# Optimization experiments

Measured on AMD Instinct MI355X. Metric: run time of the kernel, lower is better.

The kernel has to match this reference:

```python
import jax, jax.numpy as jnp
import numpy as np

D_MODEL = 1024
N_HEADS = 16
D_HEAD = D_MODEL // N_HEADS


def setup_inputs() -> dict:
    key = jax.random.key(0)
    ks = jax.random.split(key, 11)
    B, S = 2, 2048
    scale = 1.0 / np.sqrt(D_MODEL)
    inp = {
        "query": jax.random.normal(ks[0], (B, S, D_MODEL), jnp.float32),
        "key": jax.random.normal(ks[1], (B, S, D_MODEL), jnp.float32),
        "value": jax.random.normal(ks[2], (B, S, D_MODEL), jnp.float32),
        "Wq": jax.random.normal(ks[3], (D_MODEL, D_MODEL), jnp.float32) * scale,
        "bq": jnp.zeros((D_MODEL,), jnp.float32),
        "Wk": jax.random.normal(ks[4], (D_MODEL, D_MODEL), jnp.float32) * scale,
        "bk": jnp.zeros((D_MODEL,), jnp.float32),
        "Wv": jax.random.normal(ks[5], (D_MODEL, D_MODEL), jnp.float32) * scale,
        "bv": jnp.zeros((D_MODEL,), jnp.float32),
        "Wo": jax.random.normal(ks[6], (D_MODEL, D_MODEL), jnp.float32) * scale,
        "bo": jnp.zeros((D_MODEL,), jnp.float32),
    }
    return inp


def _split_heads(x):
    B, S, _ = x.shape
    return x.reshape(B, S, N_HEADS, D_HEAD).transpose(0, 2, 1, 3)  # [B,H,S,Dh]


def reference(query, key, value, Wq, bq, Wk, bk, Wv, bv, Wo, bo):
    q = _split_heads(query @ Wq + bq)
    k = _split_heads(key @ Wk + bk)
    v = _split_heads(value @ Wv + bv)
    # scores [B,H,S,S] -- faithfully materialized as in the original
    scores = jnp.einsum("bhqd,bhkd->bhqk", q, k) / np.sqrt(D_HEAD)
    attn = jax.nn.softmax(scores, axis=-1)
    out = jnp.einsum("bhqk,bhkd->bhqd", attn, v)  # [B,H,S,Dh]
    B, H, S, Dh = out.shape
    out = out.transpose(0, 2, 1, 3).reshape(B, S, H * Dh)
    return out @ Wo + bo
```

## Files before the change

kernel.cpp:

```cpp
#include <hip/hip_runtime.h>
#include <hip/hip_bf16.h>

using bf16 = __hip_bfloat16;
typedef __bf16 bf16x8 __attribute__((ext_vector_type(8)));
typedef __bf16 bf16x2v __attribute__((ext_vector_type(2)));
typedef float f32x4 __attribute__((ext_vector_type(4)));
typedef float f32x16 __attribute__((ext_vector_type(16)));

#define SEQ 2048
#define DM  1024
#define QSCALE 0.18033688011112042f

__device__ __forceinline__ f32x4 mfma16(bf16x8 a, bf16x8 b, f32x4 c) {
  return __builtin_amdgcn_mfma_f32_16x16x32_bf16(a, b, c, 0, 0, 0);
}
__device__ __forceinline__ f32x16 mfma32(bf16x8 a, bf16x8 b, f32x16 c) {
  return __builtin_amdgcn_mfma_f32_32x32x16_bf16(a, b, c, 0, 0, 0);
}
__device__ __forceinline__ void gload16(const void* g, void* l) {
  __builtin_amdgcn_global_load_lds(
      (const __attribute__((address_space(1))) unsigned int*)g,
      (__attribute__((address_space(3))) unsigned int*)l, 16, 0, 0);
}
__device__ __forceinline__ unsigned short bfbits(float x) {
  bf16 h = __float2bfloat16(x);
  return *reinterpret_cast<unsigned short*>(&h);
}
__device__ __forceinline__ unsigned pk2(float a, float b) {
#if __has_builtin(__builtin_amdgcn_cvt_pk_bf16_f32)
  bf16x2v r = __builtin_amdgcn_cvt_pk_bf16_f32(a, b);
  return *reinterpret_cast<unsigned*>(&r);
#else
  return (unsigned)bfbits(a) | ((unsigned)bfbits(b) << 16);
#endif
}
__device__ __forceinline__ float fexp2(float x) {
#if __has_builtin(__builtin_amdgcn_exp2f)
  return __builtin_amdgcn_exp2f(x);
#else
  return exp2f(x);
#endif
}
__device__ __forceinline__ void plswap(unsigned& a, unsigned& b) {
  asm("v_permlane32_swap_b32 %0, %1" : "+v"(a), "+v"(b));
}

__global__ __launch_bounds__(256) void cast_all(const float* __restrict__ q,
                                                const float* __restrict__ k,
                                                const float* __restrict__ v,
                                                const float* __restrict__ Wq,
                                                const float* __restrict__ Wk,
                                                const float* __restrict__ Wv,
                                                const float* __restrict__ Wo,
                                                bf16* __restrict__ Lx,
                                                bf16* __restrict__ Lw,
                                                bf16* __restrict__ Lwo) {
  __shared__ alignas(16) unsigned char sm[33024];
  const int t = threadIdx.x;
  if (blockIdx.y < 3) {
    const float* src = blockIdx.y == 0 ? q : (blockIdx.y == 1 ? k : v);
    const float* base = src + (size_t)blockIdx.x * 16 * 1024;
    bf16* dst = Lx + (size_t)blockIdx.y * (4096ull * 1024) + (size_t)blockIdx.x * 16384;
    bf16* const xs = (bf16*)sm;
#pragma unroll
    for (int i = 0; i < 16; ++i) {
      int u = t + i * 256;
      int row = u >> 8, c4 = u & 255;
      float4 a = *(const float4*)(base + (size_t)row * 1024 + c4 * 4);
      uint2 o;
      o.x = pk2(a.x, a.y);
      o.y = pk2(a.z, a.w);
      *(uint2*)&xs[row * 1032 + c4 * 4] = o;
    }
    __syncthreads();
#pragma unroll
    for (int i = 0; i < 8; ++i) {
      int u = t + i * 256;
      int k32 = u >> 6, l = u & 63;
      const bf16* p = &xs[(l & 15) * 1032 + k32 * 32 + (l >> 4) * 8];
      *(uint4*)(dst + (size_t)u * 8) = *(const uint4*)p;
    }
    return;
  }
  const int widx = blockIdx.y - 3;
  const float* W = widx == 0 ? Wq : (widx == 1 ? Wk : (widx == 2 ? Wv : Wo));
  bf16* dst = widx < 3 ? (Lw + (size_t)widx * 1048576) : Lwo;
  float* const tf = (float*)sm;
  const int bx = blockIdx.x & 15, by = blockIdx.x >> 4;
#pragma unroll
  for (int i = 0; i < 4; ++i) {
    int u = t + i * 256, r = u >> 4, c4 = u & 15;
    *(float4*)&tf[r * 68 + c4 * 4] = *(const float4*)(W + (size_t)(by * 64 + r) * 1024 + bx * 64 + c4 * 4);
  }
  __syncthreads();
#pragma unroll
  for (int i = 0; i < 2; ++i) {
    int u = t + i * 256;
    int sub = u >> 6, l = u & 63;
    int n16l = sub >> 1, k32l = sub & 1;
    int nn = n16l * 16 + (l & 15);
    int kk = k32l * 32 + (l >> 4) * 8;
    alignas(16) unsigned o[4];
#pragma unroll
    for (int p = 0; p < 4; ++p) o[p] = pk2(tf[(kk + 2 * p) * 68 + nn], tf[(kk + 2 * p + 1) * 68 + nn]);
    size_t off = ((((size_t)(bx * 4 + n16l)) * 32 + (by * 2 + k32l)) * 64 + l) * 8;
    *(uint4*)(dst + off) = *(const uint4*)o;
  }
}

__global__ __launch_bounds__(512, 4) void qkv_gemm(const bf16* __restrict__ Lw,
                                                   const bf16* __restrict__ Lx,
                                                   const float* __restrict__ bq,
                                                   const float* __restrict__ bk,
                                                   const float* __restrict__ bv,
                                                   bf16* __restrict__ Lq,
                                                   bf16* __restrict__ Lk,
                                                   bf16* __restrict__ Lv) {
  __shared__ alignas(16) bf16 At[2][8192];
  __shared__ alignas(16) bf16 Bt[2][4096];
  const int t = threadIdx.x, lane = t & 63, w = t >> 6;
  const int m16 = lane & 15, g4 = lane >> 4;
  const int bid = blockIdx.x;
  const int logical = (bid & 7) * 48 + (bid >> 3);
  const int third = logical >> 7;
  const int r = logical & 127;
  const int shift = third < 2 ? 5 : 3;
  const int mt = r >> shift, nt = r & ((1 << shift) - 1);
  const int wm = w >> 1, wn = w & 1;
  const bf16* Wb = Lw + (size_t)third * 1048576;
  const bf16* Xb = Lx + (size_t)third * (4096ull * 1024);
  const bf16* Asrc = third < 2 ? Wb : Xb;
  const bf16* Bsrc = third < 2 ? Xb : Wb;
  f32x4 acc[4][4] = {};

#pragma unroll
  for (int ii = 0; ii < 3; ++ii) {
    int u = w * 3 + ii;
    if (u < 16)
      gload16(Asrc + (((size_t)(mt * 16 + u) * 32 + 0) * 64 + lane) * 8, (void*)&At[0][u * 512]);
    else
      gload16(Bsrc + (((size_t)(nt * 8 + u - 16) * 32 + 0) * 64 + lane) * 8, (void*)&Bt[0][(u - 16) * 512]);
  }

  int cur = 0;
  for (int k = 0; k < 32; ++k) {
    __builtin_amdgcn_s_barrier();
    __builtin_amdgcn_sched_barrier(0);
    if (k < 31) {
      const int nb = cur ^ 1;
#pragma unroll
      for (int ii = 0; ii < 3; ++ii) {
        int u = w * 3 + ii;
        if (u < 16)
          gload16(Asrc + (((size_t)(mt * 16 + u) * 32 + k + 1) * 64 + lane) * 8, (void*)&At[nb][u * 512]);
        else
          gload16(Bsrc + (((size_t)(nt * 8 + u - 16) * 32 + k + 1) * 64 + lane) * 8,
                  (void*)&Bt[nb][(u - 16) * 512]);
      }
      asm volatile("s_waitcnt vmcnt(3)" ::: "memory");
    } else {
      asm volatile("s_waitcnt vmcnt(0)" ::: "memory");
    }
    __builtin_amdgcn_sched_barrier(0);
    __builtin_amdgcn_s_barrier();
    __builtin_amdgcn_sched_barrier(0);

    bf16x8 afr[4], bfr[4];
#pragma unroll
    for (int i = 0; i < 4; ++i) afr[i] = *(const bf16x8*)&At[cur][(wm * 4 + i) * 512 + lane * 8];
#pragma unroll
    for (int j = 0; j < 4; ++j) bfr[j] = *(const bf16x8*)&Bt[cur][(wn * 4 + j) * 512 + lane * 8];
    __builtin_amdgcn_s_setprio(1);
#pragma unroll
    for (int i = 0; i < 4; ++i)
#pragma unroll
      for (int j = 0; j < 4; ++j) acc[i][j] = mfma16(afr[i], bfr[j], acc[i][j]);
    __builtin_amdgcn_s_setprio(0);
    cur ^= 1;
  }

  if (third < 2) {
    bf16* dst = third == 0 ? Lq : Lk;
    const float* bias = third == 0 ? bq : bk;
    const float sc = third == 0 ? QSCALE : 1.0f;
#pragma unroll
    for (int mi = 0; mi < 4; ++mi) {
      int doutb = mt * 256 + wm * 64 + mi * 16 + g4 * 4;
      float4 b4 = *(const float4*)(bias + doutb);
      int hh = doutb >> 6, d32 = (doutb & 63) >> 5;
      int lhi = (doutb & 31) >> 3, half = g4 & 1;
#pragma unroll
      for (int nj = 0; nj < 4; ++nj) {
        int seq = nt * 128 + wn * 64 + nj * 16 + m16;
        int bb2 = seq >> 11, s16w = (seq & 2047) >> 4;
        size_t off = ((((size_t)(bb2 * 128 + s16w)) * 16 + hh) * 2 + d32) * 512 + (m16 + 16 * lhi) * 8 + half * 4;
        uint2 pv;
        pv.x = pk2((acc[mi][nj][0] + b4.x) * sc, (acc[mi][nj][1] + b4.y) * sc);
        pv.y = pk2((acc[mi][nj][2] + b4.z) * sc, (acc[mi][nj][3] + b4.w) * sc);
        *(uint2*)(dst + off) = pv;
      }
    }
  } else {
#pragma unroll
    for (int nj = 0; nj < 4; ++nj) {
      int dout = nt * 128 + wn * 64 + nj * 16 + m16;
      float bvv = bv[dout];
      int hh = dout >> 6, dt = (dout & 63) >> 4;
#pragma unroll
      for (int mi = 0; mi < 4; ++mi) {
        int seqb = mt * 256 + wm * 64 + mi * 16 + g4 * 4;
        int b_ = seqb >> 11, kt = (seqb & 2047) >> 6, ks32 = (seqb & 63) >> 5;
        int lhi = (seqb & 31) >> 3, half = g4 & 1;
        size_t off = (((((size_t)(b_ * 32 + kt)) * 16 + hh) * 4 + dt) * 2 + ks32) * 512 + (m16 + 16 * lhi) * 8 + half * 4;
        uint2 pv;
        pv.x = pk2(acc[mi][nj][0] + bvv, acc[mi][nj][1] + bvv);
        pv.y = pk2(acc[mi][nj][2] + bvv, acc[mi][nj][3] + bvv);
        *(uint2*)(Lv + off) = pv;
      }
    }
  }
}

__global__ __launch_bounds__(512, 4) void flash(const bf16* __restrict__ Lq,
                                                const bf16* __restrict__ Lk,
                                                const bf16* __restrict__ Lv,
                                                bf16* __restrict__ Lab) {
  __shared__ alignas(16) unsigned char smem[65536];
  bf16* const Kb = (bf16*)smem;
  bf16* const Vb = (bf16*)(smem + 32768);

  const int t = threadIdx.x, lane = t & 63, w = t >> 6;
  const int l31 = lane & 31, m16 = lane & 15, hi = lane >> 5, b4 = (lane >> 4) & 1;
  const int qw = w >> 1, g = w & 1, wg = w >> 1;
  const int bid = blockIdx.x;
  const int logical = ((bid & 7) << 6) | (bid >> 3);
  const int qt = logical & 15, h = (logical >> 4) & 15, b = logical >> 8;

  bf16x8 qf[4];
  {
    const int sQ = b * 128 + qt * 8 + qw * 2 + b4;
#pragma unroll
    for (int ks = 0; ks < 4; ++ks) {
      const int d32 = ks >> 1, g4q = (ks & 1) * 2 + hi;
      qf[ks] = *(const bf16x8*)(Lq + (((size_t)sQ * 16 + h) * 2 + d32) * 512 + (m16 + 16 * g4q) * 8);
    }
  }

  const int ss = wg >> 1, sd = wg & 1;
#pragma unroll
  for (int u = 0; u < 2; ++u) {
    const bf16* gk = Lk + ((((size_t)(b * 128 + g * 64 + u * 2 + ss)) * 16 + h) * 2 + sd) * 512 + lane * 8;
    gload16(gk, (void*)(Kb + (g * 2 + 0) * 4096 + u * 2048 + wg * 512));
    const bf16* gv = Lv + (((((size_t)(b * 32 + g * 16)) * 16 + h) * 4 + wg) * 2 + u) * 512 + lane * 8;
    gload16(gv, (void*)(Vb + (g * 2 + 0) * 4096 + u * 2048 + wg * 512));
  }

  float lrow = 0.f;
  f32x16 oacc[2] = {};
  __syncthreads();

  for (int it = 0; it < 16; ++it) {
    const int cur = it & 1;
    const bf16* const Klb = Kb + (g * 2 + cur) * 4096;
    const bf16* const Vlb = Vb + (g * 2 + cur) * 4096;
    if (it < 15) {
      const int nb = cur ^ 1;
#pragma unroll
      for (int u = 0; u < 2; ++u) {
        const int kc = (it + 1) * 2 + u;
        const bf16* gk = Lk + ((((size_t)(b * 128 + g * 64 + kc * 2 + ss)) * 16 + h) * 2 + sd) * 512 + lane * 8;
        gload16(gk, (void*)(Kb + (g * 2 + nb) * 4096 + u * 2048 + wg * 512));
        const bf16* gv = Lv + (((((size_t)(b * 32 + g * 16 + (kc >> 1))) * 16 + h) * 4 + wg) * 2 + (kc & 1)) * 512 + lane * 8;
        gload16(gv, (void*)(Vb + (g * 2 + nb) * 4096 + u * 2048 + wg * 512));
      }
    }

    f32x16 s0 = {}, s1 = {};
    __builtin_amdgcn_s_setprio(1);
#pragma unroll
    for (int ks = 0; ks < 4; ++ks) {
      const int d32 = ks >> 1, g4k = (ks & 1) * 2 + hi;
      bf16x8 kf = *(const bf16x8*)&Klb[((b4 * 2 + d32) * 64 + m16 + 16 * g4k) * 8];
      s0 = mfma32(kf, qf[ks], s0);
    }
#pragma unroll
    for (int ks = 0; ks < 4; ++ks) {
      const int d32 = ks >> 1, g4k = (ks & 1) * 2 + hi;
      bf16x8 kf = *(const bf16x8*)&Klb[2048 + ((b4 * 2 + d32) * 64 + m16 + 16 * g4k) * 8];
      s1 = mfma32(kf, qf[ks], s1);
    }
    __builtin_amdgcn_s_setprio(0);

#pragma unroll
    for (int u = 0; u < 2; ++u) {
      const bf16* const Vl = Vlb + u * 2048;
      const f32x16& s = u == 0 ? s0 : s1;
      float e[16];
#pragma unroll
      for (int r = 0; r < 16; ++r) e[r] = fexp2(s[r]);
      {
        float a0 = e[0] + e[1], a1 = e[2] + e[3], a2 = e[4] + e[5], a3 = e[6] + e[7];
        float a4 = e[8] + e[9], a5 = e[10] + e[11], a6 = e[12] + e[13], a7 = e[14] + e[15];
        lrow += ((a0 + a1) + (a2 + a3)) + ((a4 + a5) + (a6 + a7));
      }
      bf16x8 bP[2];
#pragma unroll
      for (int c = 0; c < 2; ++c) {
        unsigned P0 = pk2(e[8 * c + 0], e[8 * c + 1]);
        unsigned P1 = pk2(e[8 * c + 2], e[8 * c + 3]);
        unsigned P2 = pk2(e[8 * c + 4], e[8 * c + 5]);
        unsigned P3 = pk2(e[8 * c + 6], e[8 * c + 7]);
        plswap(P0, P2);
        plswap(P1, P3);
        alignas(16) unsigned pw[4] = {P0, P1, P2, P3};
        bP[c] = *(const bf16x8*)pw;
      }
      __builtin_amdgcn_s_setprio(1);
#pragma unroll
      for (int dtile = 0; dtile < 2; ++dtile) {
        const int dt = dtile * 2 + b4;
#pragma unroll
        for (int c = 0; c < 2; ++c) {
          bf16x8 av = *(const bf16x8*)&Vl[(dt * 64 + m16 + 16 * (2 * c + hi)) * 8];
          oacc[dtile] = mfma32(av, bP[c], oacc[dtile]);
        }
      }
      __builtin_amdgcn_s_setprio(0);
    }
    __syncthreads();
  }

  lrow += __shfl_xor(lrow, 32);

  float* const Os = (float*)smem;
  float* const Ls = (float*)(smem + 32768);
  if (g == 1) {
#pragma unroll
    for (int dtile = 0; dtile < 2; ++dtile)
#pragma unroll
      for (int r = 0; r < 16; ++r)
        Os[((qw * 2 + dtile) * 16 + r) * 64 + lane] = oacc[dtile][r];
    if (hi == 0) Ls[qw * 32 + l31] = lrow;
  }
  __syncthreads();
  if (g == 0) {
    const float inv = 1.f / (lrow + Ls[qw * 32 + l31]);
    const int sQ = b * 128 + qt * 8 + qw * 2 + b4;
#pragma unroll
    for (int dtile = 0; dtile < 2; ++dtile) {
      const int k32 = h * 2 + dtile;
#pragma unroll
      for (int j = 0; j < 8; ++j) {
        const int r = 2 * j;
        float o0 = oacc[dtile][r] + Os[((qw * 2 + dtile) * 16 + r) * 64 + lane];
        float o1 = oacc[dtile][r + 1] + Os[((qw * 2 + dtile) * 16 + r + 1) * 64 + lane];
        unsigned pv = pk2(o0 * inv, o1 * inv);
        size_t off = ((size_t)sQ * 32 + k32) * 512 + (m16 + 16 * (r >> 2)) * 8 + 4 * hi + (r & 3);
        *(unsigned*)(Lab + off) = pv;
      }
    }
  }
}

__global__ __launch_bounds__(256) void out_gemm(const bf16* __restrict__ Lab,
                                                const bf16* __restrict__ Lwo,
                                                const float* __restrict__ bo,
                                                float* __restrict__ out) {
  __shared__ alignas(16) bf16 Al[2][8192];
  __shared__ alignas(16) bf16 Bl[2][4096];
  const int t = threadIdx.x, lane = t & 63, w = t >> 6;
  const int m16 = lane & 15, g4 = lane >> 4;
  const int bid = blockIdx.y * 16 + blockIdx.x;
  const int logical = (bid & 7) * 64 + (bid >> 3);
  const int nt = logical & 15, mt = logical >> 4;
  const int wm = w >> 1, wn = w & 1;
  f32x4 acc[4][2] = {};

#pragma unroll
  for (int ii = 0; ii < 4; ++ii) {
    int s = w * 4 + ii;
    gload16(Lab + (((size_t)(mt * 8 + (s >> 1))) * 32 + (s & 1)) * 512 + lane * 8, (void*)&Al[0][s * 512]);
  }
#pragma unroll
  for (int ii = 0; ii < 2; ++ii) {
    int s = w * 2 + ii;
    gload16(Lwo + (((size_t)(nt * 4 + (s >> 1))) * 32 + (s & 1)) * 512 + lane * 8, (void*)&Bl[0][s * 512]);
  }

  int cur = 0;
  for (int slab = 0; slab < 16; ++slab) {
    __builtin_amdgcn_s_barrier();
    __builtin_amdgcn_sched_barrier(0);
    if (slab < 15) {
      const int nb = cur ^ 1, ns = slab + 1;
#pragma unroll
      for (int ii = 0; ii < 4; ++ii) {
        int s = w * 4 + ii;
        gload16(Lab + (((size_t)(mt * 8 + (s >> 1))) * 32 + ns * 2 + (s & 1)) * 512 + lane * 8,
                (void*)&Al[nb][s * 512]);
      }
#pragma unroll
      for (int ii = 0; ii < 2; ++ii) {
        int s = w * 2 + ii;
        gload16(Lwo + (((size_t)(nt * 4 + (s >> 1))) * 32 + ns * 2 + (s & 1)) * 512 + lane * 8,
                (void*)&Bl[nb][s * 512]);
      }
      asm volatile("s_waitcnt vmcnt(6)" ::: "memory");
    } else {
      asm volatile("s_waitcnt vmcnt(0)" ::: "memory");
    }
    __builtin_amdgcn_sched_barrier(0);
    __builtin_amdgcn_s_barrier();
    __builtin_amdgcn_sched_barrier(0);
#pragma unroll
    for (int c = 0; c < 2; ++c) {
      bf16x8 aA[4], bW[2];
#pragma unroll
      for (int i = 0; i < 4; ++i) aA[i] = *(const bf16x8*)&Al[cur][((wm * 4 + i) * 2 + c) * 512 + lane * 8];
#pragma unroll
      for (int j = 0; j < 2; ++j) bW[j] = *(const bf16x8*)&Bl[cur][((wn * 2 + j) * 2 + c) * 512 + lane * 8];
      __builtin_amdgcn_s_setprio(1);
#pragma unroll
      for (int i = 0; i < 4; ++i)
#pragma unroll
        for (int j = 0; j < 2; ++j) acc[i][j] = mfma16(aA[i], bW[j], acc[i][j]);
      __builtin_amdgcn_s_setprio(0);
    }
    cur ^= 1;
  }
#pragma unroll
  for (int j = 0; j < 2; ++j) {
    int n = nt * 64 + wn * 32 + j * 16 + m16;
    float bb = bo[n];
#pragma unroll
    for (int i = 0; i < 4; ++i) {
      int seqb = mt * 128 + wm * 64 + i * 16 + g4 * 4;
#pragma unroll
      for (int r = 0; r < 4; ++r) out[(size_t)(seqb + r) * 1024 + n] = acc[i][j][r] + bb;
    }
  }
}

extern "C" void kernel_launch(void* const* d_in, const int* in_sizes, int n_in,
                              void* d_out, int out_size, void* d_ws, size_t ws_size,
                              hipStream_t stream) {
  const float* query = (const float*)d_in[0];
  const float* key   = (const float*)d_in[1];
  const float* value = (const float*)d_in[2];
  const float* Wq = (const float*)d_in[3];
  const float* bq = (const float*)d_in[4];
  const float* Wk = (const float*)d_in[5];
  const float* bk = (const float*)d_in[6];
  const float* Wv = (const float*)d_in[7];
  const float* bv = (const float*)d_in[8];
  const float* Wo = (const float*)d_in[9];
  const float* bo = (const float*)d_in[10];
  float* out = (float*)d_out;

  bf16* Lw  = (bf16*)d_ws;
  bf16* Lwo = Lw + 3ull * 1048576;
  bf16* Lx  = Lwo + 1048576;
  bf16* Lq  = Lx + 3ull * 4194304;
  bf16* Lk  = Lq + 4194304;
  bf16* Lv  = Lk + 4194304;
  bf16* Lab = Lv + 4194304;

  cast_all<<<dim3(256, 7), 256, 0, stream>>>(query, key, value, Wq, Wk, Wv, Wo, Lx, Lw, Lwo);
  qkv_gemm<<<384, 512, 0, stream>>>(Lw, Lx, bq, bk, bv, Lq, Lk, Lv);
  flash<<<512, 512, 0, stream>>>(Lq, Lk, Lv, Lab);
  out_gemm<<<dim3(16, 32), 256, 0, stream>>>(Lab, Lwo, bo, out);
}
```

Measured before the change: 208.4 us.

## Compute softmax row sums with ones-MFMA and interleave QK per sub-tile

Replaces the per-lane VALU summation of exponentials and the final cross-lane shuffle with an MFMA against a bf16 ones vector, so the row sum comes from the same bf16-rounded probabilities used in the PV product. It also moves the QK score MFMAs inside the per-sub-tile loop so only one score accumulator is live at a time, which lowers register pressure. The cost is two extra MFMAs per sub-tile and a 16-register accumulator for the sums, which adds matrix-core work in exchange for less VALU work.

```diff
diff --git a/kernel.cpp b/kernel.cpp
--- a/kernel.cpp
+++ b/kernel.cpp
@@ -236,6 +236,9 @@
   const int logical = ((bid & 7) << 6) | (bid >> 3);
   const int qt = logical & 15, h = (logical >> 4) & 15, b = logical >> 8;
 
+  alignas(16) const unsigned onesw[4] = {0x3F803F80u, 0x3F803F80u, 0x3F803F80u, 0x3F803F80u};
+  const bf16x8 onesf = *(const bf16x8*)onesw;
+
   bf16x8 qf[4];
   {
     const int sQ = b * 128 + qt * 8 + qw * 2 + b4;
@@ -255,7 +258,7 @@
     gload16(gv, (void*)(Vb + (g * 2 + 0) * 4096 + u * 2048 + wg * 512));
   }
 
-  float lrow = 0.f;
+  f32x16 lacc = {};
   f32x16 oacc[2] = {};
   __syncthreads();
 
@@ -275,34 +278,24 @@
       }
     }
 
-    f32x16 s0 = {}, s1 = {};
-    __builtin_amdgcn_s_setprio(1);
-#pragma unroll
-    for (int ks = 0; ks < 4; ++ks) {
-      const int d32 = ks >> 1, g4k = (ks & 1) * 2 + hi;
-      bf16x8 kf = *(const bf16x8*)&Klb[((b4 * 2 + d32) * 64 + m16 + 16 * g4k) * 8];
-      s0 = mfma32(kf, qf[ks], s0);
-    }
-#pragma unroll
-    for (int ks = 0; ks < 4; ++ks) {
-      const int d32 = ks >> 1, g4k = (ks & 1) * 2 + hi;
-      bf16x8 kf = *(const bf16x8*)&Klb[2048 + ((b4 * 2 + d32) * 64 + m16 + 16 * g4k) * 8];
-      s1 = mfma32(kf, qf[ks], s1);
-    }
-    __builtin_amdgcn_s_setprio(0);
-
 #pragma unroll
     for (int u = 0; u < 2; ++u) {
+      const bf16* const Kl = Klb + u * 2048;
       const bf16* const Vl = Vlb + u * 2048;
-      const f32x16& s = u == 0 ? s0 : s1;
+
+      f32x16 s = {};
+      __builtin_amdgcn_s_setprio(1);
+#pragma unroll
+      for (int ks = 0; ks < 4; ++ks) {
+        const int d32 = ks >> 1, g4k = (ks & 1) * 2 + hi;
+        bf16x8 kf = *(const bf16x8*)&Kl[((b4 * 2 + d32) * 64 + m16 + 16 * g4k) * 8];
+        s = mfma32(kf, qf[ks], s);
+      }
+      __builtin_amdgcn_s_setprio(0);
+
       float e[16];
 #pragma unroll
       for (int r = 0; r < 16; ++r) e[r] = fexp2(s[r]);
-      {
-        float a0 = e[0] + e[1], a1 = e[2] + e[3], a2 = e[4] + e[5], a3 = e[6] + e[7];
-        float a4 = e[8] + e[9], a5 = e[10] + e[11], a6 = e[12] + e[13], a7 = e[14] + e[15];
-        lrow += ((a0 + a1) + (a2 + a3)) + ((a4 + a5) + (a6 + a7));
-      }
       bf16x8 bP[2];
 #pragma unroll
       for (int c = 0; c < 2; ++c) {
@@ -315,6 +308,7 @@
         alignas(16) unsigned pw[4] = {P0, P1, P2, P3};
         bP[c] = *(const bf16x8*)pw;
       }
+
       __builtin_amdgcn_s_setprio(1);
 #pragma unroll
       for (int dtile = 0; dtile < 2; ++dtile) {
@@ -325,12 +319,14 @@
           oacc[dtile] = mfma32(av, bP[c], oacc[dtile]);
         }
       }
+      lacc = mfma32(onesf, bP[0], lacc);
+      lacc = mfma32(onesf, bP[1], lacc);
       __builtin_amdgcn_s_setprio(0);
     }
     __syncthreads();
   }
 
-  lrow += __shfl_xor(lrow, 32);
+  const float lv = lacc[0];
 
   float* const Os = (float*)smem;
   float* const Ls = (float*)(smem + 32768);
@@ -340,11 +336,11 @@
 #pragma unroll
       for (int r = 0; r < 16; ++r)
         Os[((qw * 2 + dtile) * 16 + r) * 64 + lane] = oacc[dtile][r];
-    if (hi == 0) Ls[qw * 32 + l31] = lrow;
+    if (hi == 0) Ls[qw * 32 + l31] = lv;
   }
   __syncthreads();
   if (g == 0) {
-    const float inv = 1.f / (lrow + Ls[qw * 32 + l31]);
+    const float inv = 1.f / (lv + Ls[qw * 32 + l31]);
     const int sQ = b * 128 + qt * 8 + qw * 2 + b4;
 #pragma unroll
     for (int dtile = 0; dtile < 2; ++dtile) {
```

Measured after the change: 208.7 us. No clear change (+0.2%).
